# Optimization experiments

Hardware: AMD Instinct MI355X
Metric: run time of the kernel (lower is better)

Reference implementation:

```python
import jax, jax.numpy as jnp
import numpy as np

H_DIM = 1024
N_HEADS = 16
HEAD_DIM = H_DIM // N_HEADS
MAX_POS = 2048   # RotaryEmbedding default max_position_embeddings
BASE = 10000.0
SCALING_FACTOR = 1.0


def rotate_half(x):
    # interleaved convention: cat([-x[..., 1::2], x[..., ::2]], -1)
    return jnp.concatenate([-x[..., 1::2], x[..., ::2]], axis=-1)


def rope_cos_sin(seq_len, dtype):
    # LlamaDynamicNTKScalingRotaryEmbedding._set_cos_sin_cache
    base = BASE
    if seq_len > MAX_POS:
        base = BASE * (SCALING_FACTOR * seq_len / MAX_POS - (SCALING_FACTOR - 1.0)) ** (HEAD_DIM / (HEAD_DIM - 2))
    inv_freq = 1.0 / (base ** (jnp.arange(0, HEAD_DIM, 2, dtype=jnp.float32) / HEAD_DIM))
    t = jnp.arange(seq_len, dtype=jnp.float32)
    freqs = jnp.einsum('i,j->ij', t, inv_freq)          # [S, D/2]
    emb = jnp.concatenate([freqs, freqs], axis=-1)       # [S, D]
    return emb.astype(dtype), jnp.cos(emb).astype(dtype), jnp.sin(emb).astype(dtype)


def setup_inputs() -> dict:
    key = jax.random.key(0)
    ks = jax.random.split(key, 5)
    B, S = 1, 4096
    scale_w = 0.02
    return {
        'hidden_states': jax.random.normal(ks[0], (B, S, H_DIM), dtype=jnp.float32),
        'Wq': jax.random.normal(ks[1], (H_DIM, H_DIM), dtype=jnp.float32) * scale_w,
        'Wk': jax.random.normal(ks[2], (H_DIM, H_DIM), dtype=jnp.float32) * scale_w,
        'Wv': jax.random.normal(ks[3], (H_DIM, H_DIM), dtype=jnp.float32) * scale_w,
        'Wo': jax.random.normal(ks[4], (H_DIM, H_DIM), dtype=jnp.float32) * scale_w,
    }


def reference(hidden_states, Wq, Wk, Wv, Wo):
    B, S, H = hidden_states.shape
    # projections (nn.Linear: x @ W.T)
    def proj(x, W):
        y = jnp.einsum('bsh,oh->bso', x, W)
        return y.reshape(B, S, N_HEADS, HEAD_DIM).transpose(0, 2, 1, 3)  # bhsd
    q = proj(hidden_states, Wq)
    k = proj(hidden_states, Wk)
    v = proj(hidden_states, Wv)

    _, cos, sin = rope_cos_sin(S, hidden_states.dtype)
    cos = cos[None, None, :, :]   # [1,1,S,D] (position_ids = arange(S)[None], unsqueeze(1))
    sin = sin[None, None, :, :]
    q = q * cos + rotate_half(q) * sin
    k = k * cos + rotate_half(k) * sin

    # NOTE: source DIVIDES by scale = head_dim**-0.5 (i.e. multiplies by sqrt(d))
    scale = HEAD_DIM ** (-0.5)
    attn = jnp.einsum('bhsd,bhtd->bhst', q, k) / scale
    attn = jax.nn.softmax(attn, axis=-1)
    out = jnp.einsum('bhst,bhtd->bhsd', attn, v)
    out = out.transpose(0, 2, 1, 3).reshape(B, S, H)
    return jnp.einsum('bsh,oh->bso', out, Wo)
```

## Files before the change

kernel.cpp:

```cpp
#include <hip/hip_runtime.h>
#include <cmath>
#include <cstdint>

#define S_LEN 4096
#define NH 16
#define HD 64

typedef _Float16 f16x8 __attribute__((ext_vector_type(8)));
typedef __attribute__((ext_vector_type(4))) float f32x4;
typedef __attribute__((ext_vector_type(16))) float f32x16;
typedef __attribute__((ext_vector_type(4))) unsigned short u16x4;
typedef __attribute__((ext_vector_type(4))) unsigned int u32x4;
typedef int i32x2 __attribute__((ext_vector_type(2)));
typedef __attribute__((ext_vector_type(4))) float f4;

__device__ __forceinline__ unsigned short f2h(float x) {
  union { _Float16 h; unsigned short u; } v; v.h = (_Float16)x; return v.u;
}
__device__ __forceinline__ float h2f(unsigned short u) {
  union { unsigned short u; _Float16 h; } v; v.u = u; return (float)v.h;
}
__device__ __forceinline__ float exp2a(float x) {
  float r; asm("v_exp_f32 %0, %1" : "=v"(r) : "v"(x)); return r;
}
__device__ __forceinline__ unsigned pkh(float a, float b) {
  unsigned r;
  asm("v_cvt_pkrtz_f16_f32 %0, %1, %2" : "=v"(r) : "v"(a), "v"(b));
  return r;
}
__device__ __forceinline__ float max3a(float a, float b, float c) {
  float r;
  asm("v_max3_f32 %0, %1, %2, %3" : "=v"(r) : "v"(a), "v"(b), "v"(c));
  return r;
}
__device__ __forceinline__ float swapx32(float v, int hi2) {
  i32x2 r = __builtin_amdgcn_permlane32_swap(__float_as_int(v), __float_as_int(v),
                                             false, false);
  return __int_as_float(hi2 ? r[0] : r[1]);
}

#define GLL16(g, l) __builtin_amdgcn_global_load_lds( \
    (const __attribute__((address_space(1))) void*)(g), \
    (__attribute__((address_space(3))) void*)(l), 16, 0, 0)

#define PLANE_BYTES 524288
#define TILE_BYTES 8192

__global__ __launch_bounds__(256) void cvt_table_kernel(
    const float* __restrict__ hs, const float* __restrict__ wq,
    const float* __restrict__ wk, const float* __restrict__ wv,
    const float* __restrict__ wo,
    unsigned short* __restrict__ hs16,
    unsigned short* __restrict__ wq16, unsigned short* __restrict__ wk16,
    unsigned short* __restrict__ wv16, unsigned short* __restrict__ wo16,
    float* __restrict__ cosT, float* __restrict__ sinT, double base)
{
  if (blockIdx.x >= 4096) {
    int idx = (blockIdx.x - 4096) * 256 + threadIdx.x;
    if (idx < S_LEN * 32) {
      int t = idx >> 5, j = idx & 31;
      double invf = pow(base, -(double)j / 32.0);
      double f = fmod((double)t * invf, 6.283185307179586476925286766559);
      float ff = (float)f;
      cosT[idx] = cosf(ff);
      sinT[idx] = sinf(ff);
    }
    return;
  }
  const int HID4 = (S_LEN * 1024) / 4;
  const int W4   = (1024 * 1024) / 4;
  const int total = HID4 + 4 * W4;
  for (int i = blockIdx.x * 256 + threadIdx.x; i < total; i += 4096 * 256) {
    const float* s; unsigned short* d; int off;
    if (i < HID4) { s = hs; d = hs16; off = i; }
    else {
      int j = i - HID4; int w = j >> 18; off = j & (W4 - 1);
      s = (w == 0) ? wq : (w == 1) ? wk : (w == 2) ? wv : wo;
      d = (w == 0) ? wq16 : (w == 1) ? wk16 : (w == 2) ? wv16 : wo16;
    }
    f4 v = *(const f4*)(s + (size_t)off * 4);
    u16x4 r;
#pragma unroll
    for (int j = 0; j < 4; j++) r[j] = f2h(v[j]);
    *(u16x4*)(d + (size_t)off * 4) = r;
  }
}

__global__ __launch_bounds__(256) void gemm_f16(
    const unsigned short* __restrict__ A,
    const unsigned short* __restrict__ B0, const unsigned short* __restrict__ B1,
    const unsigned short* __restrict__ B2,
    void* O0, void* O1, void* O2, int M, int K, int fin)
{
  __shared__ unsigned short As[128 * 64];
  __shared__ unsigned short Bs[128 * 64];
  const int z = blockIdx.z;
  const unsigned short* B = (z == 0) ? B0 : (z == 1) ? B1 : B2;
  void* O = (z == 0) ? O0 : (z == 1) ? O1 : O2;
  const int m0 = blockIdx.y * 128, n0 = blockIdx.x * 128;
  const int tid = threadIdx.x, wid = tid >> 6, lane = tid & 63;
  const int lr = lane & 15, lk = (lane >> 4) * 8;
  const int wr = (wid >> 1) * 64, wc = (wid & 1) * 64;
  const int strow = lane >> 3;
  const int stcol = (lane & 7) * 8;

  f32x4 acc[4][4];
#pragma unroll
  for (int m = 0; m < 4; m++)
#pragma unroll
    for (int n = 0; n < 4; n++) acc[m][n] = (f32x4){0.f, 0.f, 0.f, 0.f};

  for (int kt = 0; kt < K; kt += 64) {
#pragma unroll
    for (int i = 0; i < 4; i++) {
      int c = wid * 4 + i;
      int row = c * 8 + strow;
      GLL16(A + (size_t)(m0 + row) * K + kt + stcol, &As[c * 512]);
      GLL16(B + (size_t)(n0 + row) * K + kt + stcol, &Bs[c * 512]);
    }
    __syncthreads();
    f16x8 af[4][2], bfr[4][2];
#pragma unroll
    for (int m = 0; m < 4; m++)
#pragma unroll
      for (int kk = 0; kk < 2; kk++)
        af[m][kk] = *(const f16x8*)&As[(wr + m * 16 + lr) * 64 + kk * 32 + lk];
#pragma unroll
    for (int n = 0; n < 4; n++)
#pragma unroll
      for (int kk = 0; kk < 2; kk++)
        bfr[n][kk] = *(const f16x8*)&Bs[(wc + n * 16 + lr) * 64 + kk * 32 + lk];
#pragma unroll
    for (int m = 0; m < 4; m++)
#pragma unroll
      for (int n = 0; n < 4; n++)
#pragma unroll
        for (int kk = 0; kk < 2; kk++)
          acc[m][n] = __builtin_amdgcn_mfma_f32_16x16x32_f16(
              af[m][kk], bfr[n][kk], acc[m][n], 0, 0, 0);
    __syncthreads();
  }

  const int rbase = m0 + wr + (lane >> 4) * 4;
  const int cbase = n0 + wc + lr;
  if (fin) {
    float* C = (float*)O;
#pragma unroll
    for (int m = 0; m < 4; m++)
#pragma unroll
      for (int n = 0; n < 4; n++)
#pragma unroll
        for (int j = 0; j < 4; j++) {
          int s = rbase + m * 16 + j;
          int o = cbase + n * 16;
          C[(size_t)s * 1024 + o] = acc[m][n][j];
        }
  } else if (z == 2) {
    char* base = (char*)O;
#pragma unroll
    for (int m = 0; m < 4; m++)
#pragma unroll
      for (int n = 0; n < 4; n++) {
        int s = rbase + m * 16;
        int o = cbase + n * 16;
        int hd = o >> 6, d = o & 63;
        size_t tb = (size_t)hd * PLANE_BYTES + (size_t)(s >> 6) * TILE_BYTES
                  + (size_t)d * 128;
        int cbyte = (2 * (s & 63)) ^ ((d & 7) << 4);
        u16x4 r;
#pragma unroll
        for (int j = 0; j < 4; j++) r[j] = f2h(acc[m][n][j]);
        *(u16x4*)(base + tb + cbyte) = r;
      }
  } else {
    unsigned short* C = (unsigned short*)O;
#pragma unroll
    for (int m = 0; m < 4; m++)
#pragma unroll
      for (int n = 0; n < 4; n++)
#pragma unroll
        for (int j = 0; j < 4; j++) {
          int s = rbase + m * 16 + j;
          int o = cbase + n * 16;
          C[((size_t)(o >> 6) * M + s) * HD + (o & 63)] = f2h(acc[m][n][j]);
        }
  }
}

__global__ __launch_bounds__(256) void rope_apply(
    const unsigned short* __restrict__ Qh, const unsigned short* __restrict__ Kh,
    unsigned short* __restrict__ Q16, char* __restrict__ Kt,
    const float* __restrict__ cosT, const float* __restrict__ sinT)
{
  int wid = threadIdx.x >> 6, lane = threadIdx.x & 63;
  int row = blockIdx.x * 4 + wid;
  int t = row & (S_LEN - 1);
  int head = row >> 12;
  int j = (lane < 32) ? lane : (lane - 32);
  float c = cosT[t * 32 + j], s = sinT[t * 32 + j];
  int partner = (lane < 32) ? (2 * lane + 1) : (2 * (lane - 32));
  float sgn = (lane < 32) ? -1.0f : 1.0f;
  float q = h2f(Qh[(size_t)row * HD + lane]);
  float k = h2f(Kh[(size_t)row * HD + lane]);
  float qo = __shfl(q, partner, 64);
  float ko = __shfl(k, partner, 64);
  float qr = (q * c + sgn * qo * s) * 11.541560327111707f;
  float kr = k * c + sgn * ko * s;
  Q16[(size_t)row * HD + lane] = f2h(qr);
  size_t kb = (size_t)head * PLANE_BYTES + (size_t)(t >> 6) * TILE_BYTES
            + (size_t)(t & 63) * 128 + ((2 * lane) ^ ((t & 7) << 4));
  *(unsigned short*)(Kt + kb) = f2h(kr);
}

__global__ __launch_bounds__(256, 4) void attn_kernel(
    const unsigned short* __restrict__ Q16, const char* __restrict__ Kt,
    const char* __restrict__ Vt,
    unsigned short* __restrict__ Opart, float* __restrict__ Ml)
{
  __shared__ char LDS[2][16384];

  const int tid = threadIdx.x, wid = tid >> 6, lane = tid & 63;
  const int l5 = lane & 31, hi2 = lane >> 5;
  const int z = blockIdx.z;

  int id = blockIdx.x + 32 * blockIdx.y;
  int h  = (id & 7) + 8 * ((id >> 3) & 1);
  int bx = id >> 4;
  const int qw = bx * 128 + wid * 32;

  const size_t hoff = (size_t)h * PLANE_BYTES;
  const char* KtH = Kt + hoff;
  const char* VtH = Vt + hoff;

  int aK[4];
#pragma unroll
  for (int ks = 0; ks < 4; ks++)
    aK[ks] = l5 * 128 + ((32 * ks + 16 * hi2) ^ ((l5 & 7) << 4));

  const int swid = wid * 1024;
  const int soff = swid + lane * 16;

  const unsigned short* Qrow = Q16 + ((size_t)h * S_LEN + qw + l5) * HD;
  f16x8 qf[4];
#pragma unroll
  for (int ks = 0; ks < 4; ks++)
    qf[ks] = *(const f16x8*)&Qrow[ks * 16 + hi2 * 8];

  const f32x16 zf = (f32x16)0.0f;
  f32x16 o0 = zf, o1 = zf;
  f32x16 s0, s1;
  float m_q = -__builtin_inff(), l_q = 0.f;

  const int T0 = z * 32;
  const int NT = 32;

#define STAGE(kt, B) do { \
    size_t tb = (size_t)(T0 + (kt)) * TILE_BYTES; \
    const char* gk = KtH + tb; \
    const char* gv = VtH + tb; \
    GLL16(gk + soff,        &LDS[B][swid]); \
    GLL16(gk + soff + 4096, &LDS[B][swid + 4096]); \
    GLL16(gv + soff,        &LDS[B][8192 + swid]); \
    GLL16(gv + soff + 4096, &LDS[B][8192 + swid + 4096]); \
  } while (0)

#define QKT(B) do { \
    __builtin_amdgcn_s_setprio(1); \
    _Pragma("unroll") \
    for (int ks = 0; ks < 4; ks++) { \
      f16x8 k0 = *(const f16x8*)(&LDS[B][aK[ks]]); \
      f16x8 k1 = *(const f16x8*)(&LDS[B][aK[ks] + 4096]); \
      s0 = __builtin_amdgcn_mfma_f32_32x32x16_f16(k0, qf[ks], ks ? s0 : zf, 0, 0, 0); \
      s1 = __builtin_amdgcn_mfma_f32_32x32x16_f16(k1, qf[ks], ks ? s1 : zf, 0, 0, 0); \
    } \
    __builtin_amdgcn_s_setprio(0); \
  } while (0)

#define TILE(kt, CUR, QKN, STG) do { \
    float t0 = max3a(s0[0],  s0[1],  s0[2]); \
    float t1 = max3a(s0[3],  s0[4],  s0[5]); \
    float t2 = max3a(s0[6],  s0[7],  s0[8]); \
    float t3 = max3a(s0[9],  s0[10], s0[11]); \
    float t4 = max3a(s0[12], s0[13], s0[14]); \
    float t5 = max3a(s0[15], s1[0],  s1[1]); \
    float t6 = max3a(s1[2],  s1[3],  s1[4]); \
    float t7 = max3a(s1[5],  s1[6],  s1[7]); \
    float t8 = max3a(s1[8],  s1[9],  s1[10]); \
    float t9 = max3a(s1[11], s1[12], s1[13]); \
    float ta = fmaxf(s1[14], s1[15]); \
    float u0 = max3a(t0, t1, t2); \
    float u1 = max3a(t3, t4, t5); \
    float u2 = max3a(t6, t7, t8); \
    float u3 = fmaxf(t9, ta); \
    float mx = fmaxf(max3a(u0, u1, u2), u3); \
    mx = fmaxf(mx, swapx32(mx, hi2)); \
    if (__any(mx > m_q + 11.0f)) { \
      float mnew = fmaxf(m_q, mx); \
      float alpha = exp2a(m_q - mnew); \
      m_q = mnew; \
      l_q *= alpha; \
      _Pragma("unroll") \
      for (int i = 0; i < 16; i++) { o0[i] *= alpha; o1[i] *= alpha; } \
    } \
    float rs = 0.f; \
    _Pragma("unroll") \
    for (int ks = 0; ks < 4; ks++) { \
      const int base = (ks & 1) * 8; \
      float e0, e1, e2, e3, e4, e5, e6, e7; \
      if (ks < 2) { \
        e0 = exp2a(s0[base + 0] - m_q); e1 = exp2a(s0[base + 1] - m_q); \
        e2 = exp2a(s0[base + 2] - m_q); e3 = exp2a(s0[base + 3] - m_q); \
        e4 = exp2a(s0[base + 4] - m_q); e5 = exp2a(s0[base + 5] - m_q); \
        e6 = exp2a(s0[base + 6] - m_q); e7 = exp2a(s0[base + 7] - m_q); \
      } else { \
        e0 = exp2a(s1[base + 0] - m_q); e1 = exp2a(s1[base + 1] - m_q); \
        e2 = exp2a(s1[base + 2] - m_q); e3 = exp2a(s1[base + 3] - m_q); \
        e4 = exp2a(s1[base + 4] - m_q); e5 = exp2a(s1[base + 5] - m_q); \
        e6 = exp2a(s1[base + 6] - m_q); e7 = exp2a(s1[base + 7] - m_q); \
      } \
      rs += ((e0 + e1) + (e2 + e3)) + ((e4 + e5) + (e6 + e7)); \
      unsigned a0 = pkh(e0, e1); \
      unsigned a1 = pkh(e2, e3); \
      unsigned b0 = pkh(e4, e5); \
      unsigned b1 = pkh(e6, e7); \
      i32x2 r0 = __builtin_amdgcn_permlane32_swap((int)a0, (int)b0, false, false); \
      i32x2 r1 = __builtin_amdgcn_permlane32_swap((int)a1, (int)b1, false, false); \
      u32x4 w; \
      w[0] = (unsigned)r0[0]; \
      w[1] = (unsigned)r1[0]; \
      w[2] = (unsigned)r0[1]; \
      w[3] = (unsigned)r1[1]; \
      union { u32x4 u; f16x8 f; } cv; cv.u = w; \
      f16x8 v0 = *(const f16x8*)(&LDS[CUR][aK[ks] + 8192]); \
      f16x8 v1 = *(const f16x8*)(&LDS[CUR][aK[ks] + 12288]); \
      o0 = __builtin_amdgcn_mfma_f32_32x32x16_f16(v0, cv.f, o0, 0, 0, 0); \
      o1 = __builtin_amdgcn_mfma_f32_32x32x16_f16(v1, cv.f, o1, 0, 0, 0); \
    } \
    rs += swapx32(rs, hi2); \
    l_q += rs; \
    if (QKN) { \
      asm volatile("s_waitcnt vmcnt(0)" ::: "memory"); \
      __builtin_amdgcn_s_barrier(); \
      asm volatile("" ::: "memory"); \
      QKT(CUR ^ 1); \
    } \
    if (STG) { \
      asm volatile("" ::: "memory"); \
      __builtin_amdgcn_s_barrier(); \
      asm volatile("" ::: "memory"); \
      STAGE((kt) + 2, CUR); \
    } \
  } while (0)

  STAGE(0, 0);
  asm volatile("s_waitcnt vmcnt(0)" ::: "memory");
  __builtin_amdgcn_s_barrier();
  asm volatile("" ::: "memory");
  STAGE(1, 1);
  QKT(0);

  for (int kt2 = 0; kt2 < NT - 2; kt2 += 2) {
    TILE(kt2, 0, 1, 1);
    TILE(kt2 + 1, 1, 1, 1);
  }
  TILE(NT - 2, 0, 1, 0);
  TILE(NT - 1, 1, 0, 0);
#undef STAGE
#undef QKT
#undef TILE

  const float inv = 1.0f / l_q;
  const int q = qw + l5;
  unsigned* orow = (unsigned*)(Opart + (((size_t)(z * NH + h)) * S_LEN + q) * HD);
#pragma unroll
  for (int k = 0; k < 8; k++) {
    const int d0 = 2 * (k & 1) + 8 * (k >> 1) + 4 * hi2;
    orow[d0 >> 1]        = pkh(o0[2 * k] * inv, o0[2 * k + 1] * inv);
    orow[(d0 + 32) >> 1] = pkh(o1[2 * k] * inv, o1[2 * k + 1] * inv);
  }
  if (hi2 == 0) {
    float2* mlp = (float2*)Ml + ((size_t)(z * NH + h)) * S_LEN + q;
    *mlp = make_float2(m_q, l_q);
  }
}

__global__ __launch_bounds__(256) void combine_kernel(
    const unsigned short* __restrict__ Opart, const float* __restrict__ Ml,
    unsigned short* __restrict__ Ab)
{
  const int NQ = S_LEN * 1024 / 4;
  for (int idx = blockIdx.x * 256 + threadIdx.x; idx < NQ;
       idx += gridDim.x * 256) {
    int e = idx * 4;
    int s = e >> 10;
    int col = e & 1023;
    int h = col >> 6, d = col & 63;
    const float2* mlb = (const float2*)Ml;
    float2 ml0 = mlb[(size_t)h * S_LEN + s];
    float2 ml1 = mlb[(size_t)(NH + h) * S_LEN + s];
    float mmax = fmaxf(ml0.x, ml1.x);
    float w0 = exp2f(ml0.x - mmax) * ml0.y;
    float w1 = exp2f(ml1.x - mmax) * ml1.y;
    float rden = 1.0f / (w0 + w1);
    float c0 = w0 * rden, c1 = w1 * rden;
    const unsigned short* p0 = Opart + ((size_t)h * S_LEN + s) * HD + d;
    const unsigned short* p1 = Opart + ((size_t)(NH + h) * S_LEN + s) * HD + d;
    u16x4 a = *(const u16x4*)p0;
    u16x4 b = *(const u16x4*)p1;
    u16x4 r;
#pragma unroll
    for (int j = 0; j < 4; j++)
      r[j] = f2h(c0 * h2f(a[j]) + c1 * h2f(b[j]));
    *(u16x4*)(Ab + e) = r;
  }
}

extern "C" void kernel_launch(void* const* d_in, const int* in_sizes, int n_in,
                              void* d_out, int out_size, void* d_ws, size_t ws_size,
                              hipStream_t stream)
{
  const float* hs = (const float*)d_in[0];
  const float* Wq = (const float*)d_in[1];
  const float* Wk = (const float*)d_in[2];
  const float* Wv = (const float*)d_in[3];
  const float* Wo = (const float*)d_in[4];

  char* ws = (char*)d_ws;
  const size_t HS = (size_t)S_LEN * 1024;
  const size_t WN = (size_t)1024 * 1024;
  size_t off = 0;
  unsigned short* hs16 = (unsigned short*)(ws + off); off += HS * 2;
  unsigned short* wq16 = (unsigned short*)(ws + off); off += WN * 2;
  unsigned short* wk16 = (unsigned short*)(ws + off); off += WN * 2;
  unsigned short* wv16 = (unsigned short*)(ws + off); off += WN * 2;
  unsigned short* wo16 = (unsigned short*)(ws + off); off += WN * 2;
  unsigned short* Qh16 = (unsigned short*)(ws + off); off += HS * 2;
  unsigned short* Kh16 = (unsigned short*)(ws + off); off += HS * 2;
  char* Kt_g = ws + off; off += (size_t)NH * PLANE_BYTES;
  char* VT_g = ws + off; off += (size_t)NH * PLANE_BYTES;
  unsigned short* Ab = (unsigned short*)(ws + off); off += HS * 2;
  float* Ml = (float*)(ws + off); off += (size_t)2 * NH * S_LEN * 8;
  float* cosT = (float*)(ws + off); off += (size_t)S_LEN * 32 * 4;
  float* sinT = (float*)(ws + off); off += (size_t)S_LEN * 32 * 4;
  unsigned short* Q16 = hs16;
  unsigned short* Opart = Qh16;

  double base = 10000.0 * pow((double)S_LEN / 2048.0, 64.0 / 62.0);

  cvt_table_kernel<<<4608, 256, 0, stream>>>(hs, Wq, Wk, Wv, Wo,
                                             hs16, wq16, wk16, wv16, wo16,
                                             cosT, sinT, base);

  gemm_f16<<<dim3(8, 32, 3), 256, 0, stream>>>(
      hs16, wq16, wk16, wv16, Qh16, Kh16, VT_g, S_LEN, 1024, 0);

  rope_apply<<<NH * S_LEN / 4, 256, 0, stream>>>(
      Qh16, Kh16, Q16, Kt_g, cosT, sinT);

  attn_kernel<<<dim3(32, 16, 2), 256, 0, stream>>>(
      Q16, Kt_g, VT_g, Opart, Ml);

  combine_kernel<<<2048, 256, 0, stream>>>(Opart, Ml, Ab);

  gemm_f16<<<dim3(8, 32, 1), 256, 0, stream>>>(
      Ab, wo16, wo16, wo16, d_out, d_out, d_out, S_LEN, 1024, 1);
}
```

Before: 195.9 us.

## Fuse split-KV combine into output projection GEMM prologue and raise MFMA priority

Removes the separate combine kernel and its intermediate buffer. The Wo GEMM now merges the two split-KV partial outputs while staging its A tiles, computing the per-row weights from the max/sum pairs and blending in packed f16 before writing to LDS. This saves one launch and a full write-and-read round trip of the activation buffer. In exchange, the A-tile load becomes a synchronous global load plus compute instead of an async direct-to-LDS load, and the combine weights are recomputed for every N tile. Separately, the attention kernel raises wave priority around its PV MFMAs with s_setprio.

```diff
diff --git a/kernel.cpp b/kernel.cpp
--- a/kernel.cpp
+++ b/kernel.cpp
@@ -10,6 +10,7 @@
 typedef __attribute__((ext_vector_type(4))) float f32x4;
 typedef __attribute__((ext_vector_type(16))) float f32x16;
 typedef __attribute__((ext_vector_type(4))) unsigned short u16x4;
+typedef __attribute__((ext_vector_type(8))) unsigned short u16x8;
 typedef __attribute__((ext_vector_type(4))) unsigned int u32x4;
 typedef int i32x2 __attribute__((ext_vector_type(2)));
 typedef __attribute__((ext_vector_type(4))) float f4;
@@ -31,6 +32,14 @@
 __device__ __forceinline__ float max3a(float a, float b, float c) {
   float r;
   asm("v_max3_f32 %0, %1, %2, %3" : "=v"(r) : "v"(a), "v"(b), "v"(c));
+  return r;
+}
+__device__ __forceinline__ unsigned pk_mul16(unsigned a, unsigned b) {
+  unsigned r; asm("v_pk_mul_f16 %0, %1, %2" : "=v"(r) : "v"(a), "v"(b)); return r;
+}
+__device__ __forceinline__ unsigned pk_fma16(unsigned a, unsigned b, unsigned c) {
+  unsigned r;
+  asm("v_pk_fma_f16 %0, %1, %2, %3" : "=v"(r) : "v"(a), "v"(b), "v"(c));
   return r;
 }
 __device__ __forceinline__ float swapx32(float v, int hi2) {
@@ -90,7 +99,7 @@
     const unsigned short* __restrict__ A,
     const unsigned short* __restrict__ B0, const unsigned short* __restrict__ B1,
     const unsigned short* __restrict__ B2,
-    void* O0, void* O1, void* O2, int M, int K, int fin)
+    void* O0, void* O1, void* O2, int M, int K)
 {
   __shared__ unsigned short As[128 * 64];
   __shared__ unsigned short Bs[128 * 64];
@@ -143,19 +152,7 @@
 
   const int rbase = m0 + wr + (lane >> 4) * 4;
   const int cbase = n0 + wc + lr;
-  if (fin) {
-    float* C = (float*)O;
-#pragma unroll
-    for (int m = 0; m < 4; m++)
-#pragma unroll
-      for (int n = 0; n < 4; n++)
-#pragma unroll
-        for (int j = 0; j < 4; j++) {
-          int s = rbase + m * 16 + j;
-          int o = cbase + n * 16;
-          C[(size_t)s * 1024 + o] = acc[m][n][j];
-        }
-  } else if (z == 2) {
+  if (z == 2) {
     char* base = (char*)O;
 #pragma unroll
     for (int m = 0; m < 4; m++)
@@ -185,6 +182,89 @@
           C[((size_t)(o >> 6) * M + s) * HD + (o & 63)] = f2h(acc[m][n][j]);
         }
   }
+}
+
+__global__ __launch_bounds__(256) void gemm_wo(
+    const unsigned short* __restrict__ Opart, const float* __restrict__ Ml,
+    const unsigned short* __restrict__ B,
+    float* __restrict__ Cout, int M, int K)
+{
+  __shared__ unsigned short As[128 * 64];
+  __shared__ unsigned short Bs[128 * 64];
+  const int m0 = blockIdx.y * 128, n0 = blockIdx.x * 128;
+  const int tid = threadIdx.x, wid = tid >> 6, lane = tid & 63;
+  const int lr = lane & 15, lk = (lane >> 4) * 8;
+  const int wr = (wid >> 1) * 64, wc = (wid & 1) * 64;
+  const int strow = lane >> 3;
+  const int stcol = (lane & 7) * 8;
+  const float2* mlb = (const float2*)Ml;
+
+  f32x4 acc[4][4];
+#pragma unroll
+  for (int m = 0; m < 4; m++)
+#pragma unroll
+    for (int n = 0; n < 4; n++) acc[m][n] = (f32x4){0.f, 0.f, 0.f, 0.f};
+
+  for (int kt = 0; kt < K; kt += 64) {
+    const int h = kt >> 6;
+#pragma unroll
+    for (int i = 0; i < 4; i++) {
+      int c = wid * 4 + i;
+      int row = m0 + c * 8 + strow;
+      float2 ml0 = mlb[(size_t)h * S_LEN + row];
+      float2 ml1 = mlb[(size_t)(NH + h) * S_LEN + row];
+      float mmax = fmaxf(ml0.x, ml1.x);
+      float w0 = exp2a(ml0.x - mmax) * ml0.y;
+      float w1 = exp2a(ml1.x - mmax) * ml1.y;
+      float rden = 1.0f / (w0 + w1);
+      unsigned c0p = pkh(w0 * rden, w0 * rden);
+      unsigned c1p = pkh(w1 * rden, w1 * rden);
+      const unsigned short* p0 = Opart + ((size_t)h * S_LEN + row) * HD + stcol;
+      const unsigned short* p1 = Opart + ((size_t)(NH + h) * S_LEN + row) * HD + stcol;
+      u32x4 a = *(const u32x4*)p0;
+      u32x4 b = *(const u32x4*)p1;
+      u32x4 w;
+#pragma unroll
+      for (int j = 0; j < 4; j++)
+        w[j] = pk_fma16(a[j], c0p, pk_mul16(b[j], c1p));
+      *(u32x4*)((char*)As + c * 1024 + (lane & 7) * 16 + strow * 128) = w;
+      GLL16(B + (size_t)(n0 + c * 8 + strow) * K + kt + stcol, &Bs[c * 512]);
+    }
+    __syncthreads();
+    f16x8 af[4][2], bfr[4][2];
+#pragma unroll
+    for (int m = 0; m < 4; m++)
+#pragma unroll
+      for (int kk = 0; kk < 2; kk++)
+        af[m][kk] = *(const f16x8*)&As[(wr + m * 16 + lr) * 64 + kk * 32 + lk];
+#pragma unroll
+    for (int n = 0; n < 4; n++)
+#pragma unroll
+      for (int kk = 0; kk < 2; kk++)
+        bfr[n][kk] = *(const f16x8*)&Bs[(wc + n * 16 + lr) * 64 + kk * 32 + lk];
+#pragma unroll
+    for (int m = 0; m < 4; m++)
+#pragma unroll
+      for (int n = 0; n < 4; n++)
+#pragma unroll
+        for (int kk = 0; kk < 2; kk++)
+          acc[m][n] = __builtin_amdgcn_mfma_f32_16x16x32_f16(
+              af[m][kk], bfr[n][kk], acc[m][n], 0, 0, 0);
+    __syncthreads();
+  }
+
+  const int rbase = m0 + wr + (lane >> 4) * 4;
+  const int cbase = n0 + wc + lr;
+#pragma unroll
+  for (int m = 0; m < 4; m++)
+#pragma unroll
+    for (int n = 0; n < 4; n++)
+#pragma unroll
+      for (int j = 0; j < 4; j++) {
+        int s = rbase + m * 16 + j;
+        int o = cbase + n * 16;
+        Cout[(size_t)s * 1024 + o] = acc[m][n][j];
+      }
 }
 
 __global__ __launch_bounds__(256) void rope_apply(
@@ -333,8 +413,10 @@
       union { u32x4 u; f16x8 f; } cv; cv.u = w; \
       f16x8 v0 = *(const f16x8*)(&LDS[CUR][aK[ks] + 8192]); \
       f16x8 v1 = *(const f16x8*)(&LDS[CUR][aK[ks] + 12288]); \
+      __builtin_amdgcn_s_setprio(1); \
       o0 = __builtin_amdgcn_mfma_f32_32x32x16_f16(v0, cv.f, o0, 0, 0, 0); \
       o1 = __builtin_amdgcn_mfma_f32_32x32x16_f16(v1, cv.f, o1, 0, 0, 0); \
+      __builtin_amdgcn_s_setprio(0); \
     } \
     rs += swapx32(rs, hi2); \
     l_q += rs; \
@@ -384,37 +466,6 @@
   }
 }
 
-__global__ __launch_bounds__(256) void combine_kernel(
-    const unsigned short* __restrict__ Opart, const float* __restrict__ Ml,
-    unsigned short* __restrict__ Ab)
-{
-  const int NQ = S_LEN * 1024 / 4;
-  for (int idx = blockIdx.x * 256 + threadIdx.x; idx < NQ;
-       idx += gridDim.x * 256) {
-    int e = idx * 4;
-    int s = e >> 10;
-    int col = e & 1023;
-    int h = col >> 6, d = col & 63;
-    const float2* mlb = (const float2*)Ml;
-    float2 ml0 = mlb[(size_t)h * S_LEN + s];
-    float2 ml1 = mlb[(size_t)(NH + h) * S_LEN + s];
-    float mmax = fmaxf(ml0.x, ml1.x);
-    float w0 = exp2f(ml0.x - mmax) * ml0.y;
-    float w1 = exp2f(ml1.x - mmax) * ml1.y;
-    float rden = 1.0f / (w0 + w1);
-    float c0 = w0 * rden, c1 = w1 * rden;
-    const unsigned short* p0 = Opart + ((size_t)h * S_LEN + s) * HD + d;
-    const unsigned short* p1 = Opart + ((size_t)(NH + h) * S_LEN + s) * HD + d;
-    u16x4 a = *(const u16x4*)p0;
-    u16x4 b = *(const u16x4*)p1;
-    u16x4 r;
-#pragma unroll
-    for (int j = 0; j < 4; j++)
-      r[j] = f2h(c0 * h2f(a[j]) + c1 * h2f(b[j]));
-    *(u16x4*)(Ab + e) = r;
-  }
-}
-
 extern "C" void kernel_launch(void* const* d_in, const int* in_sizes, int n_in,
                               void* d_out, int out_size, void* d_ws, size_t ws_size,
                               hipStream_t stream)
@@ -438,7 +489,6 @@
   unsigned short* Kh16 = (unsigned short*)(ws + off); off += HS * 2;
   char* Kt_g = ws + off; off += (size_t)NH * PLANE_BYTES;
   char* VT_g = ws + off; off += (size_t)NH * PLANE_BYTES;
-  unsigned short* Ab = (unsigned short*)(ws + off); off += HS * 2;
   float* Ml = (float*)(ws + off); off += (size_t)2 * NH * S_LEN * 8;
   float* cosT = (float*)(ws + off); off += (size_t)S_LEN * 32 * 4;
   float* sinT = (float*)(ws + off); off += (size_t)S_LEN * 32 * 4;
@@ -452,7 +502,7 @@
                                              cosT, sinT, base);
 
   gemm_f16<<<dim3(8, 32, 3), 256, 0, stream>>>(
-      hs16, wq16, wk16, wv16, Qh16, Kh16, VT_g, S_LEN, 1024, 0);
+      hs16, wq16, wk16, wv16, Qh16, Kh16, VT_g, S_LEN, 1024);
 
   rope_apply<<<NH * S_LEN / 4, 256, 0, stream>>>(
       Qh16, Kh16, Q16, Kt_g, cosT, sinT);
@@ -460,8 +510,6 @@
   attn_kernel<<<dim3(32, 16, 2), 256, 0, stream>>>(
       Q16, Kt_g, VT_g, Opart, Ml);
 
-  combine_kernel<<<2048, 256, 0, stream>>>(Opart, Ml, Ab);
-
-  gemm_f16<<<dim3(8, 32, 1), 256, 0, stream>>>(
-      Ab, wo16, wo16, wo16, d_out, d_out, d_out, S_LEN, 1024, 1);
-}
+  gemm_wo<<<dim3(8, 32), 256, 0, stream>>>(
+      Opart, Ml, wo16, (float*)d_out, S_LEN, 1024);
+}
```

Measured after the change: 201.3 us. 2.7% more time.
